# Optimization experiments

Hardware: AMD Instinct MI355X
Metric: run time of the kernel (lower is better)

The kernel has to match this reference:

```python
import jax, jax.numpy as jnp
import numpy as np

N = 100_000      # nodes
E = 1_600_000    # edges (avg degree 16)
D = 128          # emb_dim == hidden_dim
OUT = 128        # out_dim
NUM_BOND_TYPE = 6
NUM_BOND_DIR = 3


def _xavier(key, fan_in, fan_out, shape):
    a = np.sqrt(6.0 / (fan_in + fan_out)).astype(np.float32)
    return jax.random.uniform(key, shape, jnp.float32, -a, a)


def setup_inputs() -> dict:
    key = jax.random.key(0)
    ks = jax.random.split(key, 12)
    x = jax.random.normal(ks[0], (N, D), jnp.float32)
    edge_index = jax.random.randint(ks[1], (2, E), 0, N)
    edge_attr = jax.random.randint(ks[2], (E, 2), 0, NUM_BOND_DIR)
    # PReLU single learnable slope (torch init 0.25)
    prelu_a = jnp.full((1,), 0.25, jnp.float32)
    # enc_to_dec: Linear(D, D, bias=False), torch default uniform(-1/sqrt(D), 1/sqrt(D))
    s = 1.0 / np.sqrt(D)
    W_enc = jax.random.uniform(ks[3], (D, D), jnp.float32, -s, s)
    # edge embedding tables, xavier_uniform
    emb1 = _xavier(ks[4], NUM_BOND_TYPE, D, (NUM_BOND_TYPE, D))
    emb2 = _xavier(ks[5], NUM_BOND_DIR, D, (NUM_BOND_DIR, D))
    # GIN MLP: Linear(D, 2D) -> ReLU -> Linear(2D, OUT)
    W1 = jax.random.uniform(ks[6], (2 * D, D), jnp.float32, -s, s)
    b1 = jax.random.uniform(ks[7], (2 * D,), jnp.float32, -s, s)
    s2 = 1.0 / np.sqrt(2 * D)
    W2 = jax.random.uniform(ks[8], (OUT, 2 * D), jnp.float32, -s2, s2)
    b2 = jax.random.uniform(ks[9], (OUT,), jnp.float32, -s2, s2)
    return {
        "x": x, "edge_index": edge_index, "edge_attr": edge_attr,
        "prelu_a": prelu_a, "W_enc": W_enc,
        "emb1": emb1, "emb2": emb2,
        "W1": W1, "b1": b1, "W2": W2, "b2": b2,
    }


def reference(x, edge_index, edge_attr, prelu_a, W_enc, emb1, emb2, W1, b1, W2, b2):
    # PReLU then enc_to_dec (no bias)
    h = jnp.where(x >= 0, x, prelu_a * x)          # [N, D]
    h = h @ W_enc.T                                 # [N, D]
    src, dst = edge_index[0], edge_index[1]
    # edge embeddings for real edges
    e_emb = emb1[edge_attr[:, 0]] + emb2[edge_attr[:, 1]]  # [E, D]
    # messages: x_j + edge_attr, scatter-add at dst
    msg = h[src] + e_emb                             # [E, D]
    agg = jax.ops.segment_sum(msg, dst, num_segments=N)    # [N, D]
    # self-loops: appended edge (i, i) with attr [4, 0]
    self_emb = emb1[4] + emb2[0]                     # [D]
    agg = agg + h + self_emb[None, :]
    # GIN update MLP
    hid = jax.nn.relu(agg @ W1.T + b1)               # [N, 2D]
    out = hid @ W2.T + b2                            # [N, OUT]
    return out
```

## Files before the change

### kernel.cpp

```cpp
#include <hip/hip_runtime.h>
#include <hip/hip_bf16.h>

#define DD 128

typedef short bf16x8 __attribute__((ext_vector_type(8)));
typedef float f32x4 __attribute__((ext_vector_type(4)));

__device__ __forceinline__ float bf2f_lo(unsigned int u) {
    union { unsigned int v; float f; } x; x.v = u << 16; return x.f;
}
__device__ __forceinline__ float bf2f_hi(unsigned int u) {
    union { unsigned int v; float f; } x; x.v = u & 0xFFFF0000u; return x.f;
}
__device__ __forceinline__ unsigned short f2bf(float f) {
    union { float f; unsigned int u; } x; x.f = f;
    unsigned int u = x.u;
    unsigned int r = (u + 0x7FFFu + ((u >> 16) & 1u)) >> 16;
    return (unsigned short)r;
}

#define SBSH 7
#define SBN  128
#define NBP  256
#define NSBMAX 800
#define PKCAP 4096

__global__ __launch_bounds__(256) void sbwc_k(
    const int* __restrict__ ei, int* __restrict__ bh,
    const float* __restrict__ Wenc, const float* __restrict__ W1,
    const float* __restrict__ W2, unsigned short* __restrict__ wb,
    int E, int chunk, int nsb)
{
    __shared__ int h4[4][NSBMAX];
    const int b = blockIdx.x;
    if (b < NBP) {
        int wid = threadIdx.x >> 6;
        for (int i = threadIdx.x; i < 4 * NSBMAX; i += 256) ((int*)h4)[i] = 0;
        __syncthreads();
        int beg = b * chunk, end = min(E, beg + chunk);
        for (int e = beg + threadIdx.x; e < end; e += 256)
            atomicAdd(&h4[wid][ei[E + e] >> SBSH], 1);
        __syncthreads();
        for (int i = threadIdx.x; i < nsb; i += 256)
            bh[i * NBP + b] = h4[0][i] + h4[1][i] + h4[2][i] + h4[3][i];
        return;
    }
    int i = ((b - NBP) * 256 + threadIdx.x) * 4;
    if (i >= 81920) return;
    const float* src;
    int off;
    if (i < 16384)      { src = Wenc; off = 0; }
    else if (i < 49152) { src = W1;   off = 16384; }
    else                { src = W2;   off = 49152; }
    float4 v = *(const float4*)&src[i - off];
    ushort4 w;
    w.x = f2bf(v.x); w.y = f2bf(v.y); w.z = f2bf(v.z); w.w = f2bf(v.w);
    *(ushort4*)&wb[i] = w;
}

__global__ __launch_bounds__(256) void pscan1_k(const int* __restrict__ bh,
                                                int* __restrict__ bsum, int ntot) {
    __shared__ int ws[4];
    int base = blockIdx.x * 2048 + threadIdx.x * 8;
    int s = 0;
    #pragma unroll
    for (int i = 0; i < 8; ++i) { int idx = base + i; if (idx < ntot) s += bh[idx]; }
    int lane = threadIdx.x & 63, wid = threadIdx.x >> 6;
    int ss = s;
    #pragma unroll
    for (int o = 1; o < 64; o <<= 1) { int t = __shfl_up(ss, o, 64); if (lane >= o) ss += t; }
    if (lane == 63) ws[wid] = ss;
    __syncthreads();
    if (threadIdx.x == 0) bsum[blockIdx.x] = ws[0] + ws[1] + ws[2] + ws[3];
}

__global__ __launch_bounds__(256) void pscan3_k(const int* __restrict__ bh,
                                                const int* __restrict__ bsum,
                                                int* __restrict__ bho, int ntot) {
    __shared__ int ws[4];
    __shared__ int boff;
    const int b = blockIdx.x;
    const int t = threadIdx.x;
    const int lane = t & 63, wid = t >> 6;

    int pv = (t < b) ? bsum[t] : 0;
    #pragma unroll
    for (int o = 32; o; o >>= 1) pv += __shfl_xor(pv, o, 64);
    if (lane == 0) ws[wid] = pv;
    __syncthreads();
    if (t == 0) boff = ws[0] + ws[1] + ws[2] + ws[3];
    __syncthreads();

    int base = b * 2048 + t * 8;
    int v[8]; int s = 0;
    #pragma unroll
    for (int i = 0; i < 8; ++i) { int idx = base + i; v[i] = (idx < ntot) ? bh[idx] : 0; s += v[i]; }
    int ss = s;
    #pragma unroll
    for (int o = 1; o < 64; o <<= 1) { int u = __shfl_up(ss, o, 64); if (lane >= o) ss += u; }
    if (lane == 63) ws[wid] = ss;
    __syncthreads();
    if (t == 0) { int c = 0; for (int w = 0; w < 4; ++w) { int u = ws[w]; ws[w] = c; c += u; } }
    __syncthreads();
    int excl = ss - s + ws[wid] + boff;
    #pragma unroll
    for (int i = 0; i < 8; ++i) {
        int idx = base + i;
        if (idx < ntot) bho[idx] = excl;
        excl += v[i];
    }
}

__global__ __launch_bounds__(256) void pg_k(
    const int* __restrict__ ei, const int* __restrict__ ea,
    const int* __restrict__ bho, int* __restrict__ rec,
    const float* __restrict__ x, const unsigned short* __restrict__ Wb,
    unsigned short* __restrict__ Hb, const float* __restrict__ prelu_a,
    int E, int chunk, int nsb, int M)
{
    __shared__ int cur[NSBMAX];
    const int tid = threadIdx.x;

    if (blockIdx.x < NBP) {
        int b = blockIdx.x;
        for (int i = tid; i < nsb; i += 256) cur[i] = bho[i * NBP + b];
        __syncthreads();
        int beg = b * chunk, end = min(E, beg + chunk);
        for (int e = beg + tid; e < end; e += 256) {
            int src = ei[e];
            int dst = ei[E + e];
            int2 aa = *(const int2*)&ea[2 * e];
            int pos = atomicAdd(&cur[dst >> SBSH], 1);
            rec[pos] = src | ((aa.x * 3 + aa.y) << 17) | ((dst & (SBN - 1)) << 21);
        }
        return;
    }

    const int K = 128;
    const int wid = tid >> 6, lane = tid & 63;
    const float pa = prelu_a[0];
    const int r0 = (blockIdx.x - NBP) * 128 + wid * 32;
    const int rl = lane & 15, kb = (lane >> 4) * 8;

    bf16x8 af[2][4];
    #pragma unroll
    for (int rf = 0; rf < 2; ++rf) {
        int row = r0 + rf * 16 + rl; if (row > M - 1) row = M - 1;
        #pragma unroll
        for (int kf = 0; kf < 4; ++kf) {
            float4 v0 = *(const float4*)&x[(size_t)row * K + kf * 32 + kb];
            float4 v1 = *(const float4*)&x[(size_t)row * K + kf * 32 + kb + 4];
            v0.x = v0.x >= 0.f ? v0.x : pa * v0.x;
            v0.y = v0.y >= 0.f ? v0.y : pa * v0.y;
            v0.z = v0.z >= 0.f ? v0.z : pa * v0.z;
            v0.w = v0.w >= 0.f ? v0.w : pa * v0.w;
            v1.x = v1.x >= 0.f ? v1.x : pa * v1.x;
            v1.y = v1.y >= 0.f ? v1.y : pa * v1.y;
            v1.z = v1.z >= 0.f ? v1.z : pa * v1.z;
            v1.w = v1.w >= 0.f ? v1.w : pa * v1.w;
            bf16x8 t;
            t[0] = (short)f2bf(v0.x); t[1] = (short)f2bf(v0.y);
            t[2] = (short)f2bf(v0.z); t[3] = (short)f2bf(v0.w);
            t[4] = (short)f2bf(v1.x); t[5] = (short)f2bf(v1.y);
            t[6] = (short)f2bf(v1.z); t[7] = (short)f2bf(v1.w);
            af[rf][kf] = t;
        }
    }

    f32x4 acc[8][2];
    const f32x4 zz = {0.f, 0.f, 0.f, 0.f};
    #pragma unroll
    for (int nt = 0; nt < 8; ++nt) { acc[nt][0] = zz; acc[nt][1] = zz; }

    #pragma unroll
    for (int nt = 0; nt < 8; ++nt) {
        bf16x8 bf[4];
        #pragma unroll
        for (int kf = 0; kf < 4; ++kf)
            bf[kf] = *(const bf16x8*)&Wb[(size_t)(nt * 16 + rl) * K + kf * 32 + kb];
        #pragma unroll
        for (int rf = 0; rf < 2; ++rf)
            #pragma unroll
            for (int kf = 0; kf < 4; ++kf)
                acc[nt][rf] = __builtin_amdgcn_mfma_f32_16x16x32_bf16(af[rf][kf], bf[kf], acc[nt][rf], 0, 0, 0);
    }

    const int rq = (lane >> 4) * 4;
    #pragma unroll
    for (int nt = 0; nt < 8; ++nt) {
        int c = nt * 16 + rl;
        #pragma unroll
        for (int rf = 0; rf < 2; ++rf) {
            int rb = r0 + rf * 16 + rq;
            #pragma unroll
            for (int t = 0; t < 4; ++t) {
                int r = rb + t;
                if (r < M) Hb[(size_t)r * 128 + c] = f2bf(acc[nt][rf][t]);
            }
        }
    }
}

__global__ __launch_bounds__(1024) void csragg_k(
    const unsigned short* __restrict__ h,
    const int* __restrict__ rec,
    const int* __restrict__ bho,
    const float* __restrict__ emb1, const float* __restrict__ emb2,
    int* __restrict__ packed, unsigned int* __restrict__ aggb,
    int nsb, int M, int E)
{
    __shared__ float emb12[10][DD];
    __shared__ int hist[SBN];
    __shared__ int lstart[SBN];
    __shared__ int wsum[2];
    __shared__ int pkl[PKCAP];
    const int s = blockIdx.x;
    const int t = threadIdx.x;
    const int lane = t & 63, wid = t >> 6;

    for (int i = t; i < 10 * DD; i += 1024) {
        int c = i >> 7, col = i & 127;
        float v;
        if (c == 9) v = emb1[4 * DD + col] + emb2[col];
        else        v = emb1[(c / 3) * DD + col] + emb2[(c % 3) * DD + col];
        emb12[c][col] = v;
    }
    int sb0 = bho[s * NBP];
    int sb1 = (s == nsb - 1) ? E : bho[(s + 1) * NBP];
    if (t < SBN) hist[t] = 0;
    __syncthreads();

    const bool inlds = (sb1 - sb0) <= PKCAP;

    for (int i = sb0 + t; i < sb1; i += 1024)
        atomicAdd(&hist[(rec[i] >> 21) & (SBN - 1)], 1);
    __syncthreads();

    int v = (t < SBN) ? hist[t] : 0;
    int ss = v;
    #pragma unroll
    for (int o = 1; o < 64; o <<= 1) { int u = __shfl_up(ss, o, 64); if (lane >= o) ss += u; }
    if (t < SBN && lane == 63) wsum[wid] = ss;
    __syncthreads();
    if (t == 0) { int c = 0; for (int w = 0; w < 2; ++w) { int x2 = wsum[w]; wsum[w] = c; c += x2; } }
    __syncthreads();
    if (t < SBN) {
        lstart[t] = ss - v + wsum[wid];
        hist[t] = 0;
    }
    __syncthreads();

    if (inlds) {
        for (int i = sb0 + t; i < sb1; i += 1024) {
            int r = rec[i];
            int dl = (r >> 21) & (SBN - 1);
            int pos = lstart[dl] + atomicAdd(&hist[dl], 1);
            pkl[pos] = r & 0x1FFFFF;
        }
    } else {
        for (int i = sb0 + t; i < sb1; i += 1024) {
            int r = rec[i];
            int dl = (r >> 21) & (SBN - 1);
            int pos = sb0 + lstart[dl] + atomicAdd(&hist[dl], 1);
            packed[pos] = r & 0x1FFFFF;
        }
    }
    __syncthreads();

    const int n0 = s << SBSH;
    const int c2 = lane * 2;
    #pragma unroll
    for (int k = 0; k < SBN / 16; ++k) {
        int r = wid + k * 16;
        int n = n0 + r;
        if (n >= M) continue;
        int lbeg = lstart[r];
        int lend = lbeg + hist[r];
        unsigned int hn = *(const unsigned int*)&h[(size_t)n * DD + c2];
        float2 acc = {bf2f_lo(hn) + emb12[9][c2], bf2f_hi(hn) + emb12[9][c2 + 1]};
        if (inlds) {
            int e = lbeg;
            for (; e + 8 <= lend; e += 8) {
                int p[8]; unsigned int hv[8]; float2 m[8];
                #pragma unroll
                for (int i = 0; i < 8; ++i) p[i] = pkl[e + i];
                #pragma unroll
                for (int i = 0; i < 8; ++i)
                    hv[i] = *(const unsigned int*)&h[(size_t)(p[i] & 0x1FFFF) * DD + c2];
                #pragma unroll
                for (int i = 0; i < 8; ++i)
                    m[i] = *(const float2*)&emb12[(p[i] >> 17) & 15][c2];
                #pragma unroll
                for (int i = 0; i < 8; ++i) {
                    acc.x += bf2f_lo(hv[i]) + m[i].x;
                    acc.y += bf2f_hi(hv[i]) + m[i].y;
                }
            }
            for (; e < lend; ++e) {
                int p = pkl[e];
                unsigned int hv = *(const unsigned int*)&h[(size_t)(p & 0x1FFFF) * DD + c2];
                float2 m = *(const float2*)&emb12[(p >> 17) & 15][c2];
                acc.x += bf2f_lo(hv) + m.x;
                acc.y += bf2f_hi(hv) + m.y;
            }
        } else {
            int e = sb0 + lbeg, end = sb0 + lend;
            for (; e + 8 <= end; e += 8) {
                int p[8]; unsigned int hv[8]; float2 m[8];
                #pragma unroll
                for (int i = 0; i < 8; ++i) p[i] = packed[e + i];
                #pragma unroll
                for (int i = 0; i < 8; ++i)
                    hv[i] = *(const unsigned int*)&h[(size_t)(p[i] & 0x1FFFF) * DD + c2];
                #pragma unroll
                for (int i = 0; i < 8; ++i)
                    m[i] = *(const float2*)&emb12[(p[i] >> 17) & 15][c2];
                #pragma unroll
                for (int i = 0; i < 8; ++i) {
                    acc.x += bf2f_lo(hv[i]) + m[i].x;
                    acc.y += bf2f_hi(hv[i]) + m[i].y;
                }
            }
            for (; e < end; ++e) {
                int p = packed[e];
                unsigned int hv = *(const unsigned int*)&h[(size_t)(p & 0x1FFFF) * DD + c2];
                float2 m = *(const float2*)&emb12[(p >> 17) & 15][c2];
                acc.x += bf2f_lo(hv) + m.x;
                acc.y += bf2f_hi(hv) + m.y;
            }
        }
        aggb[((size_t)n * DD + c2) >> 1] = ((unsigned int)f2bf(acc.y) << 16) | f2bf(acc.x);
    }
}

__global__ __launch_bounds__(512) void mlp_k(
    const unsigned short* __restrict__ A,
    const unsigned short* __restrict__ w1b,
    const float* __restrict__ b1,
    const unsigned short* __restrict__ w2b,
    const float* __restrict__ b2,
    float* __restrict__ out, int M)
{
    __shared__ unsigned short W1l[256][136];
    __shared__ unsigned short hidl[128][264];
    unsigned short (*W2l)[264] = (unsigned short (*)[264])&W1l[0][0];

    const int tid = threadIdx.x;
    const int wid = tid >> 6, lane = tid & 63;
    const int rl = lane & 15, kb = (lane >> 4) * 8;
    const int rq = (lane >> 4) * 4;
    const int r0 = blockIdx.x * 128;

    #pragma unroll
    for (int idx = tid; idx < 256 * 16; idx += 512) {
        int n = idx >> 4, kq = idx & 15;
        *(ushort4*)&W1l[n][kq * 8] = *(const ushort4*)&w1b[(size_t)n * 128 + kq * 8];
        *(ushort4*)&W1l[n][kq * 8 + 4] = *(const ushort4*)&w1b[(size_t)n * 128 + kq * 8 + 4];
    }
    bf16x8 af[4];
    {
        int row = r0 + wid * 16 + rl; if (row > M - 1) row = M - 1;
        #pragma unroll
        for (int kf = 0; kf < 4; ++kf)
            af[kf] = *(const bf16x8*)&A[(size_t)row * 128 + kf * 32 + kb];
    }
    __syncthreads();

    f32x4 acc1[16];
    const f32x4 zz = {0.f, 0.f, 0.f, 0.f};
    #pragma unroll
    for (int nt = 0; nt < 16; ++nt) acc1[nt] = zz;
    #pragma unroll
    for (int nt = 0; nt < 16; ++nt) {
        bf16x8 bf[4];
        #pragma unroll
        for (int kf = 0; kf < 4; ++kf)
            bf[kf] = *(const bf16x8*)&W1l[nt * 16 + rl][kf * 32 + kb];
        #pragma unroll
        for (int kf = 0; kf < 4; ++kf)
            acc1[nt] = __builtin_amdgcn_mfma_f32_16x16x32_bf16(af[kf], bf[kf], acc1[nt], 0, 0, 0);
    }
    #pragma unroll
    for (int nt = 0; nt < 16; ++nt) {
        int c = nt * 16 + rl;
        float bi = b1[c];
        #pragma unroll
        for (int t = 0; t < 4; ++t)
            hidl[wid * 16 + rq + t][c] = f2bf(fmaxf(acc1[nt][t] + bi, 0.f));
    }
    __syncthreads();

    #pragma unroll
    for (int idx = tid; idx < 128 * 32; idx += 512) {
        int n = idx >> 5, kq = idx & 31;
        *(ushort4*)&W2l[n][kq * 8] = *(const ushort4*)&w2b[(size_t)n * 256 + kq * 8];
        *(ushort4*)&W2l[n][kq * 8 + 4] = *(const ushort4*)&w2b[(size_t)n * 256 + kq * 8 + 4];
    }
    __syncthreads();

    bf16x8 af2[8];
    #pragma unroll
    for (int kf = 0; kf < 8; ++kf)
        af2[kf] = *(const bf16x8*)&hidl[wid * 16 + rl][kf * 32 + kb];
    f32x4 acc2[8];
    #pragma unroll
    for (int nt = 0; nt < 8; ++nt) acc2[nt] = zz;
    #pragma unroll
    for (int nt = 0; nt < 8; ++nt) {
        bf16x8 bf[8];
        #pragma unroll
        for (int kf = 0; kf < 8; ++kf)
            bf[kf] = *(const bf16x8*)&W2l[nt * 16 + rl][kf * 32 + kb];
        #pragma unroll
        for (int kf = 0; kf < 8; ++kf)
            acc2[nt] = __builtin_amdgcn_mfma_f32_16x16x32_bf16(af2[kf], bf[kf], acc2[nt], 0, 0, 0);
    }
    #pragma unroll
    for (int nt = 0; nt < 8; ++nt) {
        int c = nt * 16 + rl;
        float bi = b2[c];
        #pragma unroll
        for (int t = 0; t < 4; ++t) {
            int r = r0 + wid * 16 + rq + t;
            if (r < M) out[(size_t)r * 128 + c] = acc2[nt][t] + bi;
        }
    }
}

extern "C" void kernel_launch(void* const* d_in, const int* in_sizes, int n_in,
                              void* d_out, int out_size, void* d_ws, size_t ws_size,
                              hipStream_t stream) {
    const float* x     = (const float*)d_in[0];
    const int*   ei    = (const int*)d_in[1];
    const int*   ea    = (const int*)d_in[2];
    const float* pa    = (const float*)d_in[3];
    const float* Wenc  = (const float*)d_in[4];
    const float* emb1  = (const float*)d_in[5];
    const float* emb2  = (const float*)d_in[6];
    const float* W1    = (const float*)d_in[7];
    const float* b1    = (const float*)d_in[8];
    const float* W2    = (const float*)d_in[9];
    const float* b2    = (const float*)d_in[10];
    float* out = (float*)d_out;

    const int M = in_sizes[0] / DD;
    const int E = in_sizes[1] / 2;
    const int nsb = (M + SBN - 1) >> SBSH;
    const int chunk = (E + NBP - 1) / NBP;
    const int ntot = nsb * NBP;
    const int nscb = (ntot + 2047) / 2048;

    char* ws = (char*)d_ws;
    size_t o = 0;
    unsigned short* h_bf  = (unsigned short*)(ws + o); o += (size_t)M * DD * 2;
    unsigned int*   aggb  = (unsigned int*)(ws + o);   o += (size_t)M * DD * 2;
    int* rec    = (int*)(ws + o); o += (size_t)E * 4;
    int* packed = (int*)(ws + o); o += (size_t)E * 4;
    int* bh     = (int*)(ws + o); o += (size_t)ntot * 4;
    int* bho    = (int*)(ws + o); o += (size_t)ntot * 4;
    int* bsum   = (int*)(ws + o); o += (size_t)nscb * 4;
    unsigned short* wb = (unsigned short*)(ws + o); o += 81920 * 2;
    unsigned short* wenc_b = wb;
    unsigned short* w1_b   = wb + 16384;
    unsigned short* w2_b   = wb + 49152;

    const int gm = (M + 127) / 128;
    dim3 blk(256);

    sbwc_k<<<dim3(NBP + 80), blk, 0, stream>>>(ei, bh, Wenc, W1, W2, wb, E, chunk, nsb);

    pscan1_k<<<dim3(nscb), blk, 0, stream>>>(bh, bsum, ntot);
    pscan3_k<<<dim3(nscb), blk, 0, stream>>>(bh, bsum, bho, ntot);

    pg_k<<<dim3(NBP + gm), blk, 0, stream>>>(
        ei, ea, bho, rec, x, wenc_b, h_bf, pa, E, chunk, nsb, M);

    csragg_k<<<dim3(nsb), dim3(1024), 0, stream>>>(
        h_bf, rec, bho, emb1, emb2, packed, aggb, nsb, M, E);

    mlp_k<<<dim3(gm), dim3(512), 0, stream>>>(
        (const unsigned short*)aggb, w1_b, b1, w2_b, b2, out, M);
}
```

Before: 187.2 us.

## Fuse CSR aggregation with GIN MLP in a single kernel

Merges the aggregation kernel and the two-layer MLP kernel, so each 128-node superblock's aggregated rows stay in shared memory as bf16 and feed the MFMA GEMMs directly. This removes the global write and reread of the aggregated tensor and one kernel launch. The cost is much larger shared-memory use per 1024-thread block, with W1 loaded alongside the aggregation buffers, which may lower occupancy during the gather phase. The MLP work is now split across 16 waves by row-fragment and column half.

```diff
diff --git a/kernel.cpp b/kernel.cpp
--- a/kernel.cpp
+++ b/kernel.cpp
@@ -201,23 +201,39 @@
     }
 }
 
-__global__ __launch_bounds__(1024) void csragg_k(
+__global__ __launch_bounds__(1024) void cam_k(
     const unsigned short* __restrict__ h,
     const int* __restrict__ rec,
     const int* __restrict__ bho,
     const float* __restrict__ emb1, const float* __restrict__ emb2,
-    int* __restrict__ packed, unsigned int* __restrict__ aggb,
+    int* __restrict__ packed,
+    const unsigned short* __restrict__ w1b, const float* __restrict__ b1,
+    const unsigned short* __restrict__ w2b, const float* __restrict__ b2,
+    float* __restrict__ out,
     int nsb, int M, int E)
 {
     __shared__ float emb12[10][DD];
     __shared__ int hist[SBN];
     __shared__ int lstart[SBN];
     __shared__ int wsum[2];
-    __shared__ int pkl[PKCAP];
+    __shared__ unsigned short W1l[256][136];
+    __shared__ char U[67584];
+    int* pkl = (int*)U;
+    unsigned short (*aggl)[136] = (unsigned short (*)[136])(U + 16384);
+    unsigned short (*hidl)[264] = (unsigned short (*)[264])U;
+    unsigned short (*W2l)[264] = (unsigned short (*)[264])&W1l[0][0];
+
     const int s = blockIdx.x;
     const int t = threadIdx.x;
     const int lane = t & 63, wid = t >> 6;
-
+    const int rl = lane & 15, kb = (lane >> 4) * 8;
+    const int rq = (lane >> 4) * 4;
+
+    for (int idx = t; idx < 256 * 16; idx += 1024) {
+        int n = idx >> 4, kq = idx & 15;
+        *(ushort4*)&W1l[n][kq * 8] = *(const ushort4*)&w1b[(size_t)n * 128 + kq * 8];
+        *(ushort4*)&W1l[n][kq * 8 + 4] = *(const ushort4*)&w1b[(size_t)n * 128 + kq * 8 + 4];
+    }
     for (int i = t; i < 10 * DD; i += 1024) {
         int c = i >> 7, col = i & 127;
         float v;
@@ -329,100 +345,75 @@
                 acc.y += bf2f_hi(hv) + m.y;
             }
         }
-        aggb[((size_t)n * DD + c2) >> 1] = ((unsigned int)f2bf(acc.y) << 16) | f2bf(acc.x);
-    }
-}
-
-__global__ __launch_bounds__(512) void mlp_k(
-    const unsigned short* __restrict__ A,
-    const unsigned short* __restrict__ w1b,
-    const float* __restrict__ b1,
-    const unsigned short* __restrict__ w2b,
-    const float* __restrict__ b2,
-    float* __restrict__ out, int M)
-{
-    __shared__ unsigned short W1l[256][136];
-    __shared__ unsigned short hidl[128][264];
-    unsigned short (*W2l)[264] = (unsigned short (*)[264])&W1l[0][0];
-
-    const int tid = threadIdx.x;
-    const int wid = tid >> 6, lane = tid & 63;
-    const int rl = lane & 15, kb = (lane >> 4) * 8;
-    const int rq = (lane >> 4) * 4;
-    const int r0 = blockIdx.x * 128;
-
-    #pragma unroll
-    for (int idx = tid; idx < 256 * 16; idx += 512) {
-        int n = idx >> 4, kq = idx & 15;
-        *(ushort4*)&W1l[n][kq * 8] = *(const ushort4*)&w1b[(size_t)n * 128 + kq * 8];
-        *(ushort4*)&W1l[n][kq * 8 + 4] = *(const ushort4*)&w1b[(size_t)n * 128 + kq * 8 + 4];
-    }
+        *(unsigned int*)&aggl[r][c2] = ((unsigned int)f2bf(acc.y) << 16) | f2bf(acc.x);
+    }
+    __syncthreads();
+
+    const int rf = wid & 7, ch = wid >> 3;
     bf16x8 af[4];
-    {
-        int row = r0 + wid * 16 + rl; if (row > M - 1) row = M - 1;
-        #pragma unroll
-        for (int kf = 0; kf < 4; ++kf)
-            af[kf] = *(const bf16x8*)&A[(size_t)row * 128 + kf * 32 + kb];
-    }
-    __syncthreads();
-
-    f32x4 acc1[16];
+    #pragma unroll
+    for (int kf = 0; kf < 4; ++kf)
+        af[kf] = *(const bf16x8*)&aggl[rf * 16 + rl][kf * 32 + kb];
+    __syncthreads();
+
+    f32x4 acc1[8];
     const f32x4 zz = {0.f, 0.f, 0.f, 0.f};
     #pragma unroll
-    for (int nt = 0; nt < 16; ++nt) acc1[nt] = zz;
-    #pragma unroll
-    for (int nt = 0; nt < 16; ++nt) {
+    for (int j = 0; j < 8; ++j) acc1[j] = zz;
+    #pragma unroll
+    for (int j = 0; j < 8; ++j) {
+        int nt = ch * 8 + j;
         bf16x8 bf[4];
         #pragma unroll
         for (int kf = 0; kf < 4; ++kf)
             bf[kf] = *(const bf16x8*)&W1l[nt * 16 + rl][kf * 32 + kb];
         #pragma unroll
         for (int kf = 0; kf < 4; ++kf)
-            acc1[nt] = __builtin_amdgcn_mfma_f32_16x16x32_bf16(af[kf], bf[kf], acc1[nt], 0, 0, 0);
-    }
-    #pragma unroll
-    for (int nt = 0; nt < 16; ++nt) {
-        int c = nt * 16 + rl;
+            acc1[j] = __builtin_amdgcn_mfma_f32_16x16x32_bf16(af[kf], bf[kf], acc1[j], 0, 0, 0);
+    }
+    #pragma unroll
+    for (int j = 0; j < 8; ++j) {
+        int c = (ch * 8 + j) * 16 + rl;
         float bi = b1[c];
         #pragma unroll
-        for (int t = 0; t < 4; ++t)
-            hidl[wid * 16 + rq + t][c] = f2bf(fmaxf(acc1[nt][t] + bi, 0.f));
-    }
-    __syncthreads();
-
-    #pragma unroll
-    for (int idx = tid; idx < 128 * 32; idx += 512) {
+        for (int tt = 0; tt < 4; ++tt)
+            hidl[rf * 16 + rq + tt][c] = f2bf(fmaxf(acc1[j][tt] + bi, 0.f));
+    }
+    __syncthreads();
+
+    for (int idx = t; idx < 128 * 32; idx += 1024) {
         int n = idx >> 5, kq = idx & 31;
         *(ushort4*)&W2l[n][kq * 8] = *(const ushort4*)&w2b[(size_t)n * 256 + kq * 8];
         *(ushort4*)&W2l[n][kq * 8 + 4] = *(const ushort4*)&w2b[(size_t)n * 256 + kq * 8 + 4];
     }
-    __syncthreads();
-
     bf16x8 af2[8];
     #pragma unroll
     for (int kf = 0; kf < 8; ++kf)
-        af2[kf] = *(const bf16x8*)&hidl[wid * 16 + rl][kf * 32 + kb];
-    f32x4 acc2[8];
-    #pragma unroll
-    for (int nt = 0; nt < 8; ++nt) acc2[nt] = zz;
-    #pragma unroll
-    for (int nt = 0; nt < 8; ++nt) {
+        af2[kf] = *(const bf16x8*)&hidl[rf * 16 + rl][kf * 32 + kb];
+    __syncthreads();
+
+    f32x4 acc2[4];
+    #pragma unroll
+    for (int j = 0; j < 4; ++j) acc2[j] = zz;
+    #pragma unroll
+    for (int j = 0; j < 4; ++j) {
+        int nt = ch * 4 + j;
         bf16x8 bf[8];
         #pragma unroll
         for (int kf = 0; kf < 8; ++kf)
             bf[kf] = *(const bf16x8*)&W2l[nt * 16 + rl][kf * 32 + kb];
         #pragma unroll
         for (int kf = 0; kf < 8; ++kf)
-            acc2[nt] = __builtin_amdgcn_mfma_f32_16x16x32_bf16(af2[kf], bf[kf], acc2[nt], 0, 0, 0);
-    }
-    #pragma unroll
-    for (int nt = 0; nt < 8; ++nt) {
-        int c = nt * 16 + rl;
+            acc2[j] = __builtin_amdgcn_mfma_f32_16x16x32_bf16(af2[kf], bf[kf], acc2[j], 0, 0, 0);
+    }
+    #pragma unroll
+    for (int j = 0; j < 4; ++j) {
+        int c = (ch * 4 + j) * 16 + rl;
         float bi = b2[c];
         #pragma unroll
-        for (int t = 0; t < 4; ++t) {
-            int r = r0 + wid * 16 + rq + t;
-            if (r < M) out[(size_t)r * 128 + c] = acc2[nt][t] + bi;
+        for (int tt = 0; tt < 4; ++tt) {
+            int r = n0 + rf * 16 + rq + tt;
+            if (r < M) out[(size_t)r * 128 + c] = acc2[j][tt] + bi;
         }
     }
 }
@@ -453,7 +444,6 @@
     char* ws = (char*)d_ws;
     size_t o = 0;
     unsigned short* h_bf  = (unsigned short*)(ws + o); o += (size_t)M * DD * 2;
-    unsigned int*   aggb  = (unsigned int*)(ws + o);   o += (size_t)M * DD * 2;
     int* rec    = (int*)(ws + o); o += (size_t)E * 4;
     int* packed = (int*)(ws + o); o += (size_t)E * 4;
     int* bh     = (int*)(ws + o); o += (size_t)ntot * 4;
@@ -475,9 +465,7 @@
     pg_k<<<dim3(NBP + gm), blk, 0, stream>>>(
         ei, ea, bho, rec, x, wenc_b, h_bf, pa, E, chunk, nsb, M);
 
-    csragg_k<<<dim3(nsb), dim3(1024), 0, stream>>>(
-        h_bf, rec, bho, emb1, emb2, packed, aggb, nsb, M, E);
-
-    mlp_k<<<dim3(gm), dim3(512), 0, stream>>>(
-        (const unsigned short*)aggb, w1_b, b1, w2_b, b2, out, M);
-}
+    cam_k<<<dim3(nsb), dim3(1024), 0, stream>>>(
+        h_bf, rec, bho, emb1, emb2, packed,
+        w1_b, b1, w2_b, b2, out, nsb, M, E);
+}
```

After: 204.6 us. 1.09x slower.
